# Kernel tuning notes

Hardware: AMD Instinct MI355X
Metric: run time of the kernel (lower is better)

Reference implementation:

```python
import jax, jax.numpy as jnp
import numpy as np

HIDDEN = 1024
HEADS = 16
HEAD_DIM = HIDDEN // HEADS
SCALE = 1.0 / np.sqrt(HEAD_DIM)
B, S = 2, 2048


def setup_inputs() -> dict:
    key = jax.random.key(0)
    ks = jax.random.split(key, 12)
    std = 1.0 / np.sqrt(HIDDEN)
    inp = {
        "x": jax.random.normal(ks[0], (B, S, HIDDEN), jnp.float32),
        "pos_emb": jax.random.normal(ks[1], (B, S, HIDDEN), jnp.float32),
        "mask": jnp.ones((B, S, S), jnp.int32),
        "wq": jax.random.normal(ks[2], (HIDDEN, HIDDEN), jnp.float32) * std,
        "bq": jnp.zeros((HIDDEN,), jnp.float32),
        "wk": jax.random.normal(ks[3], (HIDDEN, HIDDEN), jnp.float32) * std,
        "bk": jnp.zeros((HIDDEN,), jnp.float32),
        "wv": jax.random.normal(ks[4], (HIDDEN, HIDDEN), jnp.float32) * std,
        "bv": jnp.zeros((HIDDEN,), jnp.float32),
        "wo": jax.random.normal(ks[5], (HIDDEN, HIDDEN), jnp.float32) * std,
        "bo": jnp.zeros((HIDDEN,), jnp.float32),
        "w_pos": jax.random.normal(ks[6], (HEADS, HIDDEN), jnp.float32) * std,
    }
    return inp


def reference(x, pos_emb, mask, wq, bq, wk, bk, wv, bv, wo, bo, w_pos):
    b, s, d = x.shape
    # QKV projections (torch Linear: y = x @ W.T + b), split into heads -> (b, h, s, hd)
    q = (x @ wq.T + bq).reshape(b, s, HEADS, HEAD_DIM).transpose(0, 2, 1, 3)
    k = (x @ wk.T + bk).reshape(b, s, HEADS, HEAD_DIM).transpose(0, 2, 1, 3)
    v = (x @ wv.T + bv).reshape(b, s, HEADS, HEAD_DIM).transpose(0, 2, 1, 3)
    # learned positional bias: (b, s, heads) -> (b, heads, s), broadcast over query axis
    pos_bias = (pos_emb @ w_pos.T).transpose(0, 2, 1)  # (b, h, s_key)
    scores = jnp.einsum("bhqd,bhkd->bhqk", q, k) * SCALE
    scores = scores + pos_bias[:, :, None, :]
    scores = jnp.where(mask[:, None, :, :] == 0, -jnp.inf, scores)
    attn = jax.nn.softmax(scores.astype(jnp.float32), axis=-1).astype(q.dtype)
    # dropout p=0.0 -> identity
    out = jnp.einsum("bhqk,bhkd->bhqd", attn, v)
    out = out.transpose(0, 2, 1, 3).reshape(b, s, d)
    return out @ wo.T + bo
```

## Files before the change

kernel.cpp:

```cpp
#include <hip/hip_runtime.h>
#include <stdint.h>

typedef unsigned short u16;
typedef unsigned int u32;
typedef unsigned long long u64;
typedef __attribute__((ext_vector_type(8))) short short8;
typedef __attribute__((ext_vector_type(4))) float f32x4;

#define MFMA16(a,b,c) __builtin_amdgcn_mfma_f32_16x16x32_bf16((a),(b),(c),0,0,0)

__device__ __forceinline__ u16 f2bf(float f){
  u32 u = __builtin_bit_cast(u32, f);
  u32 r = u + 0x7FFFu + ((u >> 16) & 1u);
  return (u16)(r >> 16);
}

__device__ __forceinline__ u32 pk_bf16(float lo, float hi){
  u32 w;
  asm("v_cvt_pk_bf16_f32 %0, %1, %2" : "=v"(w) : "v"(lo), "v"(hi));
  return w;
}

__device__ __forceinline__ void gload16(const void* g, void* l){
  __builtin_amdgcn_global_load_lds((__attribute__((address_space(1))) void*)(uintptr_t)g,
                                   (__attribute__((address_space(3))) void*)l, 16, 0, 0);
}

__global__ __launch_bounds__(256) void k_prep(const float* __restrict__ x,
    const float* __restrict__ wq, const float* __restrict__ wk,
    const float* __restrict__ wv, const float* __restrict__ wo,
    const float* __restrict__ pos, const float* __restrict__ wpos,
    const int* __restrict__ mask,
    u16* __restrict__ xb, u16* __restrict__ wqb, u16* __restrict__ wkb,
    u16* __restrict__ wvb, u16* __restrict__ wob,
    float* __restrict__ posb, u64* __restrict__ pm){
  const int bx = blockIdx.x;
  if (bx < 2048){
    for (int j = bx*256 + threadIdx.x; j < 2097152; j += 2048*256){
      const float* src; u16* dst; int off;
      if (j < 1048576){ src = x; dst = xb; off = j; }
      else {
        int r = (j - 1048576) >> 18; off = (j - 1048576) & 262143;
        src = (r==0)?wq:(r==1)?wk:(r==2)?wv:wo;
        dst = (r==0)?wqb:(r==1)?wkb:(r==2)?wvb:wob;
      }
      float4 v = ((const float4*)src)[off];
      ushort4 o;
      o.x = f2bf(v.x); o.y = f2bf(v.y); o.z = f2bf(v.z); o.w = f2bf(v.w);
      ((ushort4*)dst)[off] = o;
    }
  } else if (bx < 3072){
    int row = (bx - 2048)*4 + (threadIdx.x >> 6);
    int lane = threadIdx.x & 63;
    const float* pr = pos + (size_t)row*1024;
    float pv[16];
    #pragma unroll
    for (int t=0;t<4;t++){
      float4 v = ((const float4*)pr)[lane + 64*t];
      pv[4*t+0]=v.x; pv[4*t+1]=v.y; pv[4*t+2]=v.z; pv[4*t+3]=v.w;
    }
    int b = row >> 11, s = row & 2047;
    for (int h=0; h<16; h++){
      const float* wr = wpos + h*1024;
      float acc = 0.f;
      #pragma unroll
      for (int t=0;t<4;t++){
        float4 w = ((const float4*)wr)[lane + 64*t];
        acc += pv[4*t+0]*w.x + pv[4*t+1]*w.y + pv[4*t+2]*w.z + pv[4*t+3]*w.w;
      }
      #pragma unroll
      for (int m=1;m<64;m<<=1) acc += __shfl_xor(acc, m);
      if (lane == 0) posb[(b*16 + h)*2048 + s] = acc * 1.44269504f;
    }
  } else {
    int lb = bx - 3072;
    int wi = (lb*256 + threadIdx.x) >> 6;
    int lane = threadIdx.x & 63;
    for (int w = wi; w < 131072; w += (1024*256)>>6){
      int v = mask[(size_t)w*64 + lane];
      u64 bits = __ballot(v != 0);
      if (lane == 0) pm[w] = bits;
    }
  }
}

__global__ __launch_bounds__(256) void k_qkv(const u16* __restrict__ xb,
    const u16* __restrict__ wqb, const u16* __restrict__ wkb, const u16* __restrict__ wvb,
    const float* __restrict__ bq, const float* __restrict__ bk, const float* __restrict__ bv,
    u16* __restrict__ Q, u16* __restrict__ K, u16* __restrict__ V){
  __shared__ __align__(16) u16 As[2][128*32];
  __shared__ __align__(16) u16 Bs[2][128*32];
  const int bx = blockIdx.x, by = blockIdx.y;
  const int tid = threadIdx.x, wid = tid >> 6, lane = tid & 63;
  const int wsel = by >> 3;
  const u16* W = (wsel==0) ? wqb : (wsel==1 ? wkb : wvb);
  const float* bias = (wsel==0) ? bq : (wsel==1 ? bk : bv);
  u16* dst = (wsel==0) ? Q : (wsel==1 ? K : V);
  const int m0 = bx*128, n0 = (by & 7)*128;
  const int wm = wid >> 1, wn = wid & 1;
  const int g8 = (lane >> 4)*8;

  auto stage = [&](int kt, int buf){
    #pragma unroll
    for (int jj=0;jj<2;jj++){
      int sp = wid*2 + jj;
      int p = sp*64 + lane;
      int row = p >> 2, c4 = p & 3;
      gload16(xb + (size_t)(m0+row)*1024 + kt*32 + c4*8, &As[buf][sp*512]);
      gload16(W  + (size_t)(n0+row)*1024 + kt*32 + c4*8, &Bs[buf][sp*512]);
    }
  };

  f32x4 acc[4][4];
  f32x4 z4 = {0.f,0.f,0.f,0.f};
  #pragma unroll
  for (int mf=0;mf<4;mf++)
    #pragma unroll
    for (int nf=0;nf<4;nf++) acc[mf][nf] = z4;

  stage(0, 0);
  __syncthreads();
  for (int kt=0; kt<32; kt++){
    int cur = kt & 1;
    if (kt+1 < 32) stage(kt+1, cur^1);
    short8 a[4], b[4];
    #pragma unroll
    for (int mf=0;mf<4;mf++) a[mf] = *(const short8*)&As[cur][(wm*64 + mf*16 + (lane&15))*32 + g8];
    #pragma unroll
    for (int nf=0;nf<4;nf++) b[nf] = *(const short8*)&Bs[cur][(wn*64 + nf*16 + (lane&15))*32 + g8];
    #pragma unroll
    for (int mf=0;mf<4;mf++)
      #pragma unroll
      for (int nf=0;nf<4;nf++) acc[mf][nf] = MFMA16(a[mf], b[nf], acc[mf][nf]);
    __syncthreads();
  }

  #pragma unroll
  for (int nf=0;nf<4;nf++){
    int nloc = n0 + wn*64 + nf*16 + (lane & 15);
    float bb = bias[nloc];
    int h = nloc >> 6, d = nloc & 63;
    #pragma unroll
    for (int mf=0;mf<4;mf++)
      #pragma unroll
      for (int i=0;i<4;i++){
        int m = m0 + wm*64 + mf*16 + (lane>>4)*4 + i;
        int bt = m >> 11, s = m & 2047;
        u16 val = f2bf(acc[mf][nf][i] + bb);
        if (wsel == 2)
          dst[((size_t)((bt*16 + h)*64 + d))*2048 + s] = val;
        else
          dst[((size_t)((bt*16 + h)*2048 + s))*64 + d] = val;
      }
  }
}

__global__ __launch_bounds__(256) void k_attn(const u16* __restrict__ Qg, const u16* __restrict__ Kg,
    const u16* __restrict__ Vtg, const float* __restrict__ posb, const u64* __restrict__ pmask,
    u16* __restrict__ AO){
  __shared__ __align__(16) u16 Ks[2][64*64];
  __shared__ __align__(16) u16 Vts[2][64*64];
  __shared__ __align__(16) u16 Ps[4*16*64];
  const int bid0 = blockIdx.x;
  const int bid = (bid0 & 7)*128 + (bid0 >> 3);
  const int bh = bid >> 5;
  const int qt = bid & 31;
  const int b_ = bh >> 4;
  const int h_ = bh & 15;
  const int tid = threadIdx.x, wid = tid >> 6, lane = tid & 63;
  const int g = lane >> 4, c = lane & 15;
  const int q0w = qt*64 + wid*16;
  const float SC = 0.125f * 1.44269504f;

  short8 qf0, qf1;
  {
    const u16* qp = Qg + ((size_t)(bh*2048 + q0w + c))*64 + g*8;
    qf0 = *(const short8*)qp;
    qf1 = *(const short8*)(qp + 32);
  }
  f32x4 Oa[4];
  f32x4 z4 = {0.f,0.f,0.f,0.f};
  #pragma unroll
  for (int i=0;i<4;i++) Oa[i] = z4;
  float mi[4], li[4];
  #pragma unroll
  for (int i=0;i<4;i++){ mi[i] = -1e30f; li[i] = 0.f; }

  u16* Pw = Ps + wid*1024;

  auto stage = [&](int kt, int buf){
    if (wid < 2){
      #pragma unroll
      for (int jj=0;jj<4;jj++){
        int sx = wid*4 + jj;
        int p = sx*64 + lane;
        int r = p >> 3, o16 = p & 7;
        int tau = 2*(r&15) + ((r>>4)&1) + (r&32);
        gload16(Kg + ((size_t)(bh*2048 + kt*64 + tau))*64 + (o16 ^ (r&7))*8, &Ks[buf][sx*512]);
      }
    } else {
      #pragma unroll
      for (int jj=0;jj<4;jj++){
        int sv = (wid-2)*4 + jj;
        int p = sv*64 + lane;
        int d = p >> 3, o16 = p & 7;
        gload16(Vtg + ((size_t)(bh*64 + d))*2048 + kt*64 + (o16 ^ (d&7))*8, &Vts[buf][sv*512]);
      }
    }
  };

  stage(0, 0);
  __syncthreads();

  for (int kt=0; kt<32; kt++){
    const int cur = kt & 1;
    if (kt+1 < 32) stage(kt+1, cur^1);

    f32x4 sc[4];
    #pragma unroll
    for (int nf=0;nf<4;nf++) sc[nf] = z4;
    __builtin_amdgcn_s_setprio(1);
    #pragma unroll
    for (int ks=0;ks<2;ks++){
      short8 qf = ks ? qf1 : qf0;
      #pragma unroll
      for (int nf=0;nf<4;nf++){
        int r = nf*16 + c;
        unsigned off = (unsigned)(r*128 + ks*64 + g*16) ^ (unsigned)((r&7)<<4);
        short8 kb = *(const short8*)((const char*)&Ks[cur][0] + off);
        sc[nf] = MFMA16(qf, kb, sc[nf]);
      }
    }
    __builtin_amdgcn_s_setprio(0);

    float2 pb01 = *(const float2*)&posb[bh*2048 + kt*64 + 2*c];
    float2 pb23 = *(const float2*)&posb[bh*2048 + kt*64 + 32 + 2*c];
    u64 mw[4];
    #pragma unroll
    for (int i=0;i<4;i++) mw[i] = pmask[((size_t)(b_*2048 + q0w + g*4 + i))*32 + kt];

    float pv_[4][4], lmax[4];
    #pragma unroll
    for (int i=0;i<4;i++){
      pv_[0][i] = sc[0][i]*SC + pb01.x;
      pv_[1][i] = sc[1][i]*SC + pb01.y;
      pv_[2][i] = sc[2][i]*SC + pb23.x;
      pv_[3][i] = sc[3][i]*SC + pb23.y;
      u64 m = mw[i];
      if (m != ~0ull){
        u32 lo = (u32)(m >> (2*c));
        u32 hi = (u32)(m >> (2*c + 32));
        if (!(lo & 1u)) pv_[0][i] = -1e30f;
        if (!(lo & 2u)) pv_[1][i] = -1e30f;
        if (!(hi & 1u)) pv_[2][i] = -1e30f;
        if (!(hi & 2u)) pv_[3][i] = -1e30f;
      }
      lmax[i] = fmaxf(fmaxf(pv_[0][i], pv_[1][i]), fmaxf(pv_[2][i], pv_[3][i]));
    }
    float need = fmaxf(fmaxf(lmax[0]-mi[0], lmax[1]-mi[1]),
                       fmaxf(lmax[2]-mi[2], lmax[3]-mi[3]));
    if (__any(need > 8.0f)){
      #pragma unroll
      for (int i=0;i<4;i++){
        float t = lmax[i];
        t = fmaxf(t, __shfl_xor(t, 1));
        t = fmaxf(t, __shfl_xor(t, 2));
        t = fmaxf(t, __shfl_xor(t, 4));
        t = fmaxf(t, __shfl_xor(t, 8));
        float mn = fmaxf(mi[i], t);
        float al = __builtin_amdgcn_exp2f(mi[i] - mn);
        mi[i] = mn;
        li[i] *= al;
        #pragma unroll
        for (int db=0;db<4;db++) Oa[db][i] *= al;
      }
    }
    #pragma unroll
    for (int i=0;i<4;i++){
      float rs = 0.f;
      #pragma unroll
      for (int nf=0;nf<4;nf++){
        float e = __builtin_amdgcn_exp2f(pv_[nf][i] - mi[i]);
        pv_[nf][i] = e;
        rs += e;
      }
      li[i] += rs;
    }

    #pragma unroll
    for (int i=0;i<4;i++){
      int qr = g*4 + i;
      u32 w0 = pk_bf16(pv_[0][i], pv_[1][i]);
      u32 w1 = pk_bf16(pv_[2][i], pv_[3][i]);
      unsigned o0 = (unsigned)(qr*128 + 4*c) ^ (unsigned)((qr&7)<<4);
      unsigned o1 = (unsigned)(qr*128 + 64 + 4*c) ^ (unsigned)((qr&7)<<4);
      *(u32*)((char*)Pw + o0) = w0;
      *(u32*)((char*)Pw + o1) = w1;
    }

    __builtin_amdgcn_s_setprio(1);
    #pragma unroll
    for (int ks=0;ks<2;ks++){
      unsigned aoff = (unsigned)(c*128 + ks*64 + g*16) ^ (unsigned)((c&7)<<4);
      short8 pa = *(const short8*)((const char*)Pw + aoff);
      #pragma unroll
      for (int db=0;db<4;db++){
        int d = db*16 + c;
        unsigned boff = (unsigned)(d*128 + ks*64 + g*16) ^ (unsigned)((d&7)<<4);
        short8 vb = *(const short8*)((const char*)&Vts[cur][0] + boff);
        Oa[db] = MFMA16(pa, vb, Oa[db]);
      }
    }
    __builtin_amdgcn_s_setprio(0);
    __syncthreads();
  }

  #pragma unroll
  for (int i=0;i<4;i++){
    float s = li[i];
    s += __shfl_xor(s, 1);
    s += __shfl_xor(s, 2);
    s += __shfl_xor(s, 4);
    s += __shfl_xor(s, 8);
    float inv = 1.0f / s;
    int q = q0w + g*4 + i;
    size_t base = ((size_t)(b_*2048 + q))*1024 + h_*64;
    #pragma unroll
    for (int db=0;db<4;db++)
      AO[base + db*16 + c] = f2bf(Oa[db][i] * inv);
  }
}

__global__ __launch_bounds__(256) void k_out(const u16* __restrict__ A, const u16* __restrict__ W,
    const float* __restrict__ bo, float* __restrict__ out){
  __shared__ __align__(16) u16 As[2][128*32];
  __shared__ __align__(16) u16 Bs[2][128*32];
  const int bx = blockIdx.x, by = blockIdx.y;
  const int tid = threadIdx.x, wid = tid >> 6, lane = tid & 63;
  const int m0 = bx*128, n0 = by*128;
  const int wm = wid >> 1, wn = wid & 1;
  const int g8 = (lane >> 4)*8;

  auto stage = [&](int kt, int buf){
    #pragma unroll
    for (int jj=0;jj<2;jj++){
      int sp = wid*2 + jj;
      int p = sp*64 + lane;
      int row = p >> 2, c4 = p & 3;
      gload16(A + (size_t)(m0+row)*1024 + kt*32 + c4*8, &As[buf][sp*512]);
      gload16(W + (size_t)(n0+row)*1024 + kt*32 + c4*8, &Bs[buf][sp*512]);
    }
  };

  f32x4 acc[4][4];
  f32x4 z4 = {0.f,0.f,0.f,0.f};
  #pragma unroll
  for (int mf=0;mf<4;mf++)
    #pragma unroll
    for (int nf=0;nf<4;nf++) acc[mf][nf] = z4;

  stage(0, 0);
  __syncthreads();
  for (int kt=0; kt<32; kt++){
    int cur = kt & 1;
    if (kt+1 < 32) stage(kt+1, cur^1);
    short8 a[4], b[4];
    #pragma unroll
    for (int mf=0;mf<4;mf++) a[mf] = *(const short8*)&As[cur][(wm*64 + mf*16 + (lane&15))*32 + g8];
    #pragma unroll
    for (int nf=0;nf<4;nf++) b[nf] = *(const short8*)&Bs[cur][(wn*64 + nf*16 + (lane&15))*32 + g8];
    #pragma unroll
    for (int mf=0;mf<4;mf++)
      #pragma unroll
      for (int nf=0;nf<4;nf++) acc[mf][nf] = MFMA16(a[mf], b[nf], acc[mf][nf]);
    __syncthreads();
  }

  #pragma unroll
  for (int nf=0;nf<4;nf++){
    int n = n0 + wn*64 + nf*16 + (lane & 15);
    float bb = bo[n];
    #pragma unroll
    for (int mf=0;mf<4;mf++)
      #pragma unroll
      for (int i=0;i<4;i++){
        int m = m0 + wm*64 + mf*16 + (lane>>4)*4 + i;
        out[(size_t)m*1024 + n] = acc[mf][nf][i] + bb;
      }
  }
}

extern "C" void kernel_launch(void* const* d_in, const int* in_sizes, int n_in,
                              void* d_out, int out_size, void* d_ws, size_t ws_size,
                              hipStream_t stream){
  const float* x    = (const float*)d_in[0];
  const float* pos  = (const float*)d_in[1];
  const int*   mask = (const int*)d_in[2];
  const float* wq   = (const float*)d_in[3];
  const float* bq   = (const float*)d_in[4];
  const float* wk   = (const float*)d_in[5];
  const float* bk   = (const float*)d_in[6];
  const float* wv   = (const float*)d_in[7];
  const float* bv   = (const float*)d_in[8];
  const float* wo   = (const float*)d_in[9];
  const float* bo   = (const float*)d_in[10];
  const float* wpos = (const float*)d_in[11];
  float* out = (float*)d_out;

  char* ws = (char*)d_ws;
  u16* xb   = (u16*)(ws);
  u16* wqb  = (u16*)(ws + ((size_t)8  << 20));
  u16* wkb  = (u16*)(ws + ((size_t)10 << 20));
  u16* wvb  = (u16*)(ws + ((size_t)12 << 20));
  u16* wob  = (u16*)(ws + ((size_t)14 << 20));
  u16* Qb   = (u16*)(ws + ((size_t)16 << 20));
  u16* Kb   = (u16*)(ws + ((size_t)24 << 20));
  u16* Vtb  = (u16*)(ws + ((size_t)32 << 20));
  u16* AO   = (u16*)(ws + ((size_t)40 << 20));
  float* posb = (float*)(ws + ((size_t)48 << 20));
  u64* pm   = (u64*)(ws + ((size_t)49 << 20));

  k_prep<<<dim3(4096), dim3(256), 0, stream>>>(x, wq, wk, wv, wo, pos, wpos, mask,
                                               xb, wqb, wkb, wvb, wob, posb, pm);
  k_qkv<<<dim3(32,24), dim3(256), 0, stream>>>(xb, wqb, wkb, wvb, bq, bk, bv, Qb, Kb, Vtb);
  k_attn<<<dim3(1024), dim3(256), 0, stream>>>(Qb, Kb, Vtb, posb, pm, AO);
  k_out<<<dim3(32,8), dim3(256), 0, stream>>>(AO, wob, bo, out);
}
```

Measured before the change: 312.1 us.

## Double attention query tile per wave to reuse K/V fragments across two rows

Each wave in the attention kernel now processes 32 query rows (two 16-row MFMA fragments) instead of 16, so every block covers 128 queries and the grid halves to 512 blocks. K and V tiles loaded from LDS are reused across both query fragments, which halves K/V global staging traffic and LDS reads per query. In exchange register pressure roughly doubles for accumulators and softmax state, and with only 512 blocks on the device occupancy and load balance may suffer.

After: 294.6 us. 1.06x faster.

```diff
diff --git a/kernel.cpp b/kernel.cpp
--- a/kernel.cpp
+++ b/kernel.cpp
@@ -160,33 +160,38 @@
     u16* __restrict__ AO){
   __shared__ __align__(16) u16 Ks[2][64*64];
   __shared__ __align__(16) u16 Vts[2][64*64];
-  __shared__ __align__(16) u16 Ps[4*16*64];
+  __shared__ __align__(16) u16 Ps[4][32*64];
   const int bid0 = blockIdx.x;
-  const int bid = (bid0 & 7)*128 + (bid0 >> 3);
-  const int bh = bid >> 5;
-  const int qt = bid & 31;
+  const int bid = (bid0 & 7)*64 + (bid0 >> 3);
+  const int bh = bid >> 4;
+  const int qt = bid & 15;
   const int b_ = bh >> 4;
   const int h_ = bh & 15;
   const int tid = threadIdx.x, wid = tid >> 6, lane = tid & 63;
   const int g = lane >> 4, c = lane & 15;
-  const int q0w = qt*64 + wid*16;
+  const int q0w = qt*128 + wid*32;
   const float SC = 0.125f * 1.44269504f;
 
-  short8 qf0, qf1;
-  {
-    const u16* qp = Qg + ((size_t)(bh*2048 + q0w + c))*64 + g*8;
-    qf0 = *(const short8*)qp;
-    qf1 = *(const short8*)(qp + 32);
-  }
-  f32x4 Oa[4];
+  short8 qf[2][2];
+  #pragma unroll
+  for (int mf=0;mf<2;mf++){
+    const u16* qp = Qg + ((size_t)(bh*2048 + q0w + mf*16 + c))*64 + g*8;
+    qf[mf][0] = *(const short8*)qp;
+    qf[mf][1] = *(const short8*)(qp + 32);
+  }
+  f32x4 Oa[2][4];
   f32x4 z4 = {0.f,0.f,0.f,0.f};
   #pragma unroll
-  for (int i=0;i<4;i++) Oa[i] = z4;
-  float mi[4], li[4];
-  #pragma unroll
-  for (int i=0;i<4;i++){ mi[i] = -1e30f; li[i] = 0.f; }
-
-  u16* Pw = Ps + wid*1024;
+  for (int mf=0;mf<2;mf++)
+    #pragma unroll
+    for (int db=0;db<4;db++) Oa[mf][db] = z4;
+  float mi[2][4], li[2][4];
+  #pragma unroll
+  for (int mf=0;mf<2;mf++)
+    #pragma unroll
+    for (int i=0;i<4;i++){ mi[mf][i] = -1e30f; li[mf][i] = 0.f; }
+
+  u16* Pw = Ps[wid];
 
   auto stage = [&](int kt, int buf){
     if (wid < 2){
@@ -216,99 +221,126 @@
     const int cur = kt & 1;
     if (kt+1 < 32) stage(kt+1, cur^1);
 
-    f32x4 sc[4];
-    #pragma unroll
-    for (int nf=0;nf<4;nf++) sc[nf] = z4;
+    f32x4 sc[2][4];
+    #pragma unroll
+    for (int mf=0;mf<2;mf++)
+      #pragma unroll
+      for (int nf=0;nf<4;nf++) sc[mf][nf] = z4;
     __builtin_amdgcn_s_setprio(1);
     #pragma unroll
     for (int ks=0;ks<2;ks++){
-      short8 qf = ks ? qf1 : qf0;
+      short8 kb[4];
       #pragma unroll
       for (int nf=0;nf<4;nf++){
         int r = nf*16 + c;
         unsigned off = (unsigned)(r*128 + ks*64 + g*16) ^ (unsigned)((r&7)<<4);
-        short8 kb = *(const short8*)((const char*)&Ks[cur][0] + off);
-        sc[nf] = MFMA16(qf, kb, sc[nf]);
-      }
+        kb[nf] = *(const short8*)((const char*)&Ks[cur][0] + off);
+      }
+      #pragma unroll
+      for (int nf=0;nf<4;nf++)
+        #pragma unroll
+        for (int mf=0;mf<2;mf++)
+          sc[mf][nf] = MFMA16(qf[mf][ks], kb[nf], sc[mf][nf]);
     }
     __builtin_amdgcn_s_setprio(0);
 
     float2 pb01 = *(const float2*)&posb[bh*2048 + kt*64 + 2*c];
     float2 pb23 = *(const float2*)&posb[bh*2048 + kt*64 + 32 + 2*c];
-    u64 mw[4];
-    #pragma unroll
-    for (int i=0;i<4;i++) mw[i] = pmask[((size_t)(b_*2048 + q0w + g*4 + i))*32 + kt];
-
-    float pv_[4][4], lmax[4];
-    #pragma unroll
-    for (int i=0;i<4;i++){
-      pv_[0][i] = sc[0][i]*SC + pb01.x;
-      pv_[1][i] = sc[1][i]*SC + pb01.y;
-      pv_[2][i] = sc[2][i]*SC + pb23.x;
-      pv_[3][i] = sc[3][i]*SC + pb23.y;
-      u64 m = mw[i];
-      if (m != ~0ull){
-        u32 lo = (u32)(m >> (2*c));
-        u32 hi = (u32)(m >> (2*c + 32));
-        if (!(lo & 1u)) pv_[0][i] = -1e30f;
-        if (!(lo & 2u)) pv_[1][i] = -1e30f;
-        if (!(hi & 1u)) pv_[2][i] = -1e30f;
-        if (!(hi & 2u)) pv_[3][i] = -1e30f;
-      }
-      lmax[i] = fmaxf(fmaxf(pv_[0][i], pv_[1][i]), fmaxf(pv_[2][i], pv_[3][i]));
-    }
-    float need = fmaxf(fmaxf(lmax[0]-mi[0], lmax[1]-mi[1]),
-                       fmaxf(lmax[2]-mi[2], lmax[3]-mi[3]));
+    u64 mw[2][4];
+    #pragma unroll
+    for (int mf=0;mf<2;mf++)
+      #pragma unroll
+      for (int i=0;i<4;i++)
+        mw[mf][i] = pmask[((size_t)(b_*2048 + q0w + mf*16 + g*4 + i))*32 + kt];
+
+    float pv_[2][4][4], lmax[2][4];
+    #pragma unroll
+    for (int mf=0;mf<2;mf++)
+      #pragma unroll
+      for (int i=0;i<4;i++){
+        pv_[mf][0][i] = sc[mf][0][i]*SC + pb01.x;
+        pv_[mf][1][i] = sc[mf][1][i]*SC + pb01.y;
+        pv_[mf][2][i] = sc[mf][2][i]*SC + pb23.x;
+        pv_[mf][3][i] = sc[mf][3][i]*SC + pb23.y;
+        u64 m = mw[mf][i];
+        if (m != ~0ull){
+          u32 lo = (u32)(m >> (2*c));
+          u32 hi = (u32)(m >> (2*c + 32));
+          if (!(lo & 1u)) pv_[mf][0][i] = -1e30f;
+          if (!(lo & 2u)) pv_[mf][1][i] = -1e30f;
+          if (!(hi & 1u)) pv_[mf][2][i] = -1e30f;
+          if (!(hi & 2u)) pv_[mf][3][i] = -1e30f;
+        }
+        lmax[mf][i] = fmaxf(fmaxf(pv_[mf][0][i], pv_[mf][1][i]),
+                            fmaxf(pv_[mf][2][i], pv_[mf][3][i]));
+      }
+    float need = -1e30f;
+    #pragma unroll
+    for (int mf=0;mf<2;mf++)
+      #pragma unroll
+      for (int i=0;i<4;i++) need = fmaxf(need, lmax[mf][i] - mi[mf][i]);
     if (__any(need > 8.0f)){
       #pragma unroll
+      for (int mf=0;mf<2;mf++)
+        #pragma unroll
+        for (int i=0;i<4;i++){
+          float t = lmax[mf][i];
+          t = fmaxf(t, __shfl_xor(t, 1));
+          t = fmaxf(t, __shfl_xor(t, 2));
+          t = fmaxf(t, __shfl_xor(t, 4));
+          t = fmaxf(t, __shfl_xor(t, 8));
+          float mn = fmaxf(mi[mf][i], t);
+          float al = __builtin_amdgcn_exp2f(mi[mf][i] - mn);
+          mi[mf][i] = mn;
+          li[mf][i] *= al;
+          #pragma unroll
+          for (int db=0;db<4;db++) Oa[mf][db][i] *= al;
+        }
+    }
+    #pragma unroll
+    for (int mf=0;mf<2;mf++)
+      #pragma unroll
       for (int i=0;i<4;i++){
-        float t = lmax[i];
-        t = fmaxf(t, __shfl_xor(t, 1));
-        t = fmaxf(t, __shfl_xor(t, 2));
-        t = fmaxf(t, __shfl_xor(t, 4));
-        t = fmaxf(t, __shfl_xor(t, 8));
-        float mn = fmaxf(mi[i], t);
-        float al = __builtin_amdgcn_exp2f(mi[i] - mn);
-        mi[i] = mn;
-        li[i] *= al;
+        float rs = 0.f;
         #pragma unroll
-        for (int db=0;db<4;db++) Oa[db][i] *= al;
-      }
-    }
-    #pragma unroll
-    for (int i=0;i<4;i++){
-      float rs = 0.f;
-      #pragma unroll
-      for (int nf=0;nf<4;nf++){
-        float e = __builtin_amdgcn_exp2f(pv_[nf][i] - mi[i]);
-        pv_[nf][i] = e;
-        rs += e;
-      }
-      li[i] += rs;
-    }
-
-    #pragma unroll
-    for (int i=0;i<4;i++){
-      int qr = g*4 + i;
-      u32 w0 = pk_bf16(pv_[0][i], pv_[1][i]);
-      u32 w1 = pk_bf16(pv_[2][i], pv_[3][i]);
-      unsigned o0 = (unsigned)(qr*128 + 4*c) ^ (unsigned)((qr&7)<<4);
-      unsigned o1 = (unsigned)(qr*128 + 64 + 4*c) ^ (unsigned)((qr&7)<<4);
-      *(u32*)((char*)Pw + o0) = w0;
-      *(u32*)((char*)Pw + o1) = w1;
-    }
+        for (int nf=0;nf<4;nf++){
+          float e = __builtin_amdgcn_exp2f(pv_[mf][nf][i] - mi[mf][i]);
+          pv_[mf][nf][i] = e;
+          rs += e;
+        }
+        li[mf][i] += rs;
+      }
+
+    #pragma unroll
+    for (int mf=0;mf<2;mf++)
+      #pragma unroll
+      for (int i=0;i<4;i++){
+        int qr = mf*16 + g*4 + i;
+        u32 w0 = pk_bf16(pv_[mf][0][i], pv_[mf][1][i]);
+        u32 w1 = pk_bf16(pv_[mf][2][i], pv_[mf][3][i]);
+        unsigned o0 = (unsigned)(qr*128 + 4*c) ^ (unsigned)((qr&7)<<4);
+        unsigned o1 = (unsigned)(qr*128 + 64 + 4*c) ^ (unsigned)((qr&7)<<4);
+        *(u32*)((char*)Pw + o0) = w0;
+        *(u32*)((char*)Pw + o1) = w1;
+      }
 
     __builtin_amdgcn_s_setprio(1);
     #pragma unroll
     for (int ks=0;ks<2;ks++){
-      unsigned aoff = (unsigned)(c*128 + ks*64 + g*16) ^ (unsigned)((c&7)<<4);
-      short8 pa = *(const short8*)((const char*)Pw + aoff);
+      short8 pa[2];
+      #pragma unroll
+      for (int mf=0;mf<2;mf++){
+        unsigned aoff = (unsigned)((mf*16 + c)*128 + ks*64 + g*16) ^ (unsigned)((c&7)<<4);
+        pa[mf] = *(const short8*)((const char*)Pw + aoff);
+      }
       #pragma unroll
       for (int db=0;db<4;db++){
         int d = db*16 + c;
         unsigned boff = (unsigned)(d*128 + ks*64 + g*16) ^ (unsigned)((d&7)<<4);
         short8 vb = *(const short8*)((const char*)&Vts[cur][0] + boff);
-        Oa[db] = MFMA16(pa, vb, Oa[db]);
+        #pragma unroll
+        for (int mf=0;mf<2;mf++)
+          Oa[mf][db] = MFMA16(pa[mf], vb, Oa[mf][db]);
       }
     }
     __builtin_amdgcn_s_setprio(0);
@@ -316,19 +348,21 @@
   }
 
   #pragma unroll
-  for (int i=0;i<4;i++){
-    float s = li[i];
-    s += __shfl_xor(s, 1);
-    s += __shfl_xor(s, 2);
-    s += __shfl_xor(s, 4);
-    s += __shfl_xor(s, 8);
-    float inv = 1.0f / s;
-    int q = q0w + g*4 + i;
-    size_t base = ((size_t)(b_*2048 + q))*1024 + h_*64;
-    #pragma unroll
-    for (int db=0;db<4;db++)
-      AO[base + db*16 + c] = f2bf(Oa[db][i] * inv);
-  }
+  for (int mf=0;mf<2;mf++)
+    #pragma unroll
+    for (int i=0;i<4;i++){
+      float s = li[mf][i];
+      s += __shfl_xor(s, 1);
+      s += __shfl_xor(s, 2);
+      s += __shfl_xor(s, 4);
+      s += __shfl_xor(s, 8);
+      float inv = 1.0f / s;
+      int q = q0w + mf*16 + g*4 + i;
+      size_t base = ((size_t)(b_*2048 + q))*1024 + h_*64;
+      #pragma unroll
+      for (int db=0;db<4;db++)
+        AO[base + db*16 + c] = f2bf(Oa[mf][db][i] * inv);
+    }
 }
 
 __global__ __launch_bounds__(256) void k_out(const u16* __restrict__ A, const u16* __restrict__ W,
@@ -423,6 +457,6 @@
   k_prep<<<dim3(4096), dim3(256), 0, stream>>>(x, wq, wk, wv, wo, pos, wpos, mask,
                                                xb, wqb, wkb, wvb, wob, posb, pm);
   k_qkv<<<dim3(32,24), dim3(256), 0, stream>>>(xb, wqb, wkb, wvb, bq, bk, bv, Qb, Kb, Vtb);
-  k_attn<<<dim3(1024), dim3(256), 0, stream>>>(Qb, Kb, Vtb, posb, pm, AO);
+  k_attn<<<dim3(512), dim3(256), 0, stream>>>(Qb, Kb, Vtb, posb, pm, AO);
   k_out<<<dim3(32,8), dim3(256), 0, stream>>>(AO, wob, bo, out);
 }
```
